# Kernel optimization log

Measured on AMD Instinct MI355X. Metric: run time of the kernel, lower is better.

Reference implementation:

```python
import jax, jax.numpy as jnp
import numpy as np

# angular momenta of the full basis (2s,3s,2p,3p,3d) -> block sizes 1,1,3,3,5; norb=13
L_LIST = [0, 0, 1, 1, 2]


def factor_matrix():
    """Replicates the orbital-pair loop: factor 0.5 on diagonal orbital blocks,
    1.0 for i<j blocks, 0.0 below the block diagonal (only i<=j filled)."""
    sizes = [2 * l + 1 for l in L_LIST]
    norb = sum(sizes)
    F = np.zeros((norb, norb), np.float32)
    ist = 0
    for i, si in enumerate(sizes):
        jst = 0
        for j, sj in enumerate(sizes):
            if i < j:
                F[ist:ist + si, jst:jst + sj] = 1.0
            elif i == j:
                F[ist:ist + si, jst:jst + sj] = 0.5
            jst += sj
        ist += si
    return jnp.asarray(F)


def setup_inputs() -> dict:
    key = jax.random.key(0)
    k1, k2, k3, k4, k5 = jax.random.split(key, 5)
    N, E, K = 128, 2048, 16
    norb = sum(2 * l + 1 for l in L_LIST)  # 13
    return {
        "hopping": jax.random.normal(k1, (E, norb * norb), jnp.float32),
        "onsite": jax.random.normal(k2, (N, norb * norb), jnp.float32),
        "kpoints": jax.random.uniform(k3, (K, 3), jnp.float32),
        "cell_shift": jax.random.normal(k4, (E, 3), jnp.float32),
        "edge_index": jax.random.randint(k5, (2, E), 0, N, jnp.int64),
    }


def reference(hopping, onsite, kpoints, cell_shift, edge_index):
    F = factor_matrix()
    norb = F.shape[0]
    N = onsite.shape[0]
    K = kpoints.shape[0]
    ctype = jnp.complex64

    # per-edge / per-atom orbital blocks with upper-triangular factor (i<=j loop)
    hop = (hopping.reshape(-1, norb, norb) * F).astype(ctype)   # [E,norb,norb]
    ons = (onsite.reshape(-1, norb, norb) * F).astype(ctype)    # [N,norb,norb]

    # Bloch phase exp(-i 2*pi k.R) per (k, edge)
    phase = jnp.exp(-1j * 2.0 * jnp.pi * (kpoints @ cell_shift.T).astype(ctype))  # [K,E]

    # assemble block Hamiltonian [K, N, N, norb, norb]
    H = jnp.zeros((K, N, N, norb, norb), ctype)
    ar = jnp.arange(N)
    H = H.at[:, ar, ar].add(ons[None])  # onsite diagonal blocks (no phase)
    ie, je = edge_index[0], edge_index[1]
    H = H.at[:, ie, je].add(phase[:, :, None, None] * hop[None])  # scatter-add edges

    # hermitize: block + block^H (swap atom blocks and orbital indices)
    H = H + jnp.conj(jnp.swapaxes(jnp.swapaxes(H, 1, 2), 3, 4))
    # [K, N, norb, N, norb] -> [K, all_norb, all_norb]
    Hk = H.transpose(0, 1, 3, 2, 4).reshape(K, N * norb, N * norb)
    return Hk
```

## Files before the change

kernel.cpp:

```cpp
#include <hip/hip_runtime.h>
#include <math.h>

#define NORB 13
#define NORB2 (NORB * NORB)
#define GB 16
#define NCOL (GB * NORB)
#define KSPLIT 2
#define MAXE 128
#define NTHR 256

typedef float fx2 __attribute__((ext_vector_type(2)));

__device__ __forceinline__ int blk_of(int p) {
    return p < 1 ? 0 : (p < 2 ? 1 : (p < 5 ? 2 : (p < 8 ? 3 : 4)));
}
__device__ __forceinline__ float bfac(int bp, int bq) {
    return bp < bq ? 1.0f : (bp == bq ? 0.5f : 0.0f);
}

__global__ void __launch_bounds__(NTHR)
k_fused(const float* __restrict__ hopping,
        const float* __restrict__ onsite,
        const float* __restrict__ kpoints,
        const float* __restrict__ cell_shift,
        const int* __restrict__ edge_index,
        float* __restrict__ out,
        int N, int E, int K, int ld, int es, int ngroups) {
    int g  = blockIdx.x % ngroups;
    int a  = (blockIdx.x / ngroups) % N;
    int kc = blockIdx.x / (ngroups * N);
    int kch = (K + KSPLIT - 1) / KSPLIT;
    int k0 = kc * kch, k1 = min(K, k0 + kch);
    int tid = threadIdx.x;
    int b0 = g * GB;

    __shared__ int ecnt;
    __shared__ int list[MAXE];

    if (tid == 0) ecnt = 0;
    __syncthreads();

    for (int e = tid; e < E; e += NTHR) {
        int ie = edge_index[e], je = edge_index[E + e];
        if (ie == a && (je >> 4) == g) {
            int pos = atomicAdd(&ecnt, 1);
            if (pos < MAXE) list[pos] = (e << 5) | ((je & 15) << 1);
        }
        if (je == a && (ie >> 4) == g) {
            int pos = atomicAdd(&ecnt, 1);
            if (pos < MAXE) list[pos] = (e << 5) | ((ie & 15) << 1) | 1;
        }
    }
    __syncthreads();
    int nent = min(__builtin_amdgcn_readfirstlane(ecnt), MAXE);

    int lane = tid & 63;
    int myent = (lane < nent) ? list[lane] : 0;

    int c = tid;
    if (c >= NCOL || g * NCOL + c >= ld) return;
    int i_c = c / NORB;
    int q   = c - i_c * NORB;
    int bq  = blk_of(q);
    bool diagact = (b0 + i_c == a);
    const float* on = onsite + (size_t)a * NORB2;

    for (int k = k0; k < k1; ++k) {
        float kx = kpoints[3 * k], ky = kpoints[3 * k + 1], kz = kpoints[3 * k + 2];

        float ax[NORB], ay[NORB];
        #pragma unroll
        for (int p = 0; p < NORB; ++p) {
            float v = 0.f;
            if (diagact) {
                int bp = blk_of(p);
                v = on[p * NORB + q] * bfac(bp, bq)
                  + on[q * NORB + p] * bfac(bq, bp);
            }
            ax[p] = v; ay[p] = 0.f;
        }

        for (int it = 0; it < nent; ++it) {
            int ent = (it < 64) ? __builtin_amdgcn_readlane(myent, it) : list[it];
            int e = ent >> 5;
            int islot = (ent >> 1) & 15;
            int rev = ent & 1;
            const float* cs = cell_shift + 3 * (size_t)e;
            float d = kx * cs[0] + ky * cs[1] + kz * cs[2];
            float s, cc;
            __sincosf(-6.2831853071795864f * d, &s, &cc);
            float sv = rev ? -s : s;
            if (i_c == islot) {
                const float* h = hopping + (size_t)e * NORB2;
                if (rev) {
                    #pragma unroll
                    for (int p = 0; p < NORB; ++p) {
                        float hv = h[q * NORB + p] * bfac(bq, blk_of(p));
                        ax[p] += cc * hv; ay[p] += sv * hv;
                    }
                } else {
                    #pragma unroll
                    for (int p = 0; p < NORB; ++p) {
                        float hv = h[p * NORB + q] * bfac(blk_of(p), bq);
                        ax[p] += cc * hv; ay[p] += sv * hv;
                    }
                }
            }
        }

        size_t base = ((size_t)(k * ld + a * NORB)) * ld + (size_t)g * NCOL + c;
        if (es == 2) {
            fx2* o2 = (fx2*)out;
            #pragma unroll
            for (int p = 0; p < NORB; ++p)
                o2[base + (size_t)p * ld] = (fx2){ax[p], ay[p]};
        } else {
            #pragma unroll
            for (int p = 0; p < NORB; ++p)
                out[base + (size_t)p * ld] = ax[p];
        }
    }
}

extern "C" void kernel_launch(void* const* d_in, const int* in_sizes, int n_in,
                              void* d_out, int out_size, void* d_ws, size_t ws_size,
                              hipStream_t stream) {
    const float* hopping    = (const float*)d_in[0];
    const float* onsite     = (const float*)d_in[1];
    const float* kpoints    = (const float*)d_in[2];
    const float* cell_shift = (const float*)d_in[3];
    const int*   edge_index = (const int*)d_in[4];
    float* out = (float*)d_out;

    int E = in_sizes[0] / NORB2;
    int N = in_sizes[1] / NORB2;
    int K = in_sizes[2] / 3;
    int ld = N * NORB;
    int ngroups = (N + GB - 1) / GB;

    size_t full = (size_t)K * ld * ld * 2;
    int es = ((size_t)out_size >= full) ? 2 : 1;

    int nwg = N * ngroups * KSPLIT;
    k_fused<<<nwg, NTHR, 0, stream>>>(hopping, onsite, kpoints, cell_shift,
                                      edge_index, out, N, E, K, ld, es, ngroups);
}
```

Before: 207.9 us.

## Map one workgroup per (k, atom) row with two columns per thread

Reorganises the grid so each workgroup of 832 threads handles a full block-row for one k-point and atom, with each thread owning two adjacent output columns. Phases are computed once per edge into shared memory instead of per thread per edge, and stores become 16-byte vector writes of two complex values. This removes the per-column-group edge rescans and redundant sincos work, at the cost of more registers per thread and larger workgroups.

```diff
diff --git a/kernel.cpp b/kernel.cpp
--- a/kernel.cpp
+++ b/kernel.cpp
@@ -3,13 +3,11 @@
 
 #define NORB 13
 #define NORB2 (NORB * NORB)
-#define GB 16
-#define NCOL (GB * NORB)
-#define KSPLIT 2
-#define MAXE 128
-#define NTHR 256
+#define NTHR 832
+#define MAXE 256
 
 typedef float fx2 __attribute__((ext_vector_type(2)));
+typedef float fx4 __attribute__((ext_vector_type(4)));
 
 __device__ __forceinline__ int blk_of(int p) {
     return p < 1 ? 0 : (p < 2 ? 1 : (p < 5 ? 2 : (p < 8 ? 3 : 4)));
@@ -25,99 +23,112 @@
         const float* __restrict__ cell_shift,
         const int* __restrict__ edge_index,
         float* __restrict__ out,
-        int N, int E, int K, int ld, int es, int ngroups) {
-    int g  = blockIdx.x % ngroups;
-    int a  = (blockIdx.x / ngroups) % N;
-    int kc = blockIdx.x / (ngroups * N);
-    int kch = (K + KSPLIT - 1) / KSPLIT;
-    int k0 = kc * kch, k1 = min(K, k0 + kch);
+        int N, int E, int K, int ld, int es) {
+    int a = blockIdx.x % N;
+    int k = blockIdx.x / N;
     int tid = threadIdx.x;
-    int b0 = g * GB;
 
     __shared__ int ecnt;
-    __shared__ int list[MAXE];
+    __shared__ int   elist[MAXE];
+    __shared__ float phc[MAXE];
+    __shared__ float phs[MAXE];
 
     if (tid == 0) ecnt = 0;
     __syncthreads();
 
     for (int e = tid; e < E; e += NTHR) {
         int ie = edge_index[e], je = edge_index[E + e];
-        if (ie == a && (je >> 4) == g) {
-            int pos = atomicAdd(&ecnt, 1);
-            if (pos < MAXE) list[pos] = (e << 5) | ((je & 15) << 1);
-        }
-        if (je == a && (ie >> 4) == g) {
-            int pos = atomicAdd(&ecnt, 1);
-            if (pos < MAXE) list[pos] = (e << 5) | ((ie & 15) << 1) | 1;
-        }
+        if (ie == a) { int pos = atomicAdd(&ecnt, 1);
+                       if (pos < MAXE) elist[pos] = (e << 8) | (je << 1); }
+        if (je == a) { int pos = atomicAdd(&ecnt, 1);
+                       if (pos < MAXE) elist[pos] = (e << 8) | (ie << 1) | 1; }
     }
     __syncthreads();
     int nent = min(__builtin_amdgcn_readfirstlane(ecnt), MAXE);
 
+    float kx = kpoints[3 * k], ky = kpoints[3 * k + 1], kz = kpoints[3 * k + 2];
+    for (int t = tid; t < nent; t += NTHR) {
+        int ent = elist[t];
+        int e = ent >> 8;
+        float d = kx * cell_shift[3 * e] + ky * cell_shift[3 * e + 1]
+                + kz * cell_shift[3 * e + 2];
+        float s, c;
+        __sincosf(-6.2831853071795864f * d, &s, &c);
+        phc[t] = c;
+        phs[t] = (ent & 1) ? -s : s;
+    }
+    __syncthreads();
+
     int lane = tid & 63;
-    int myent = (lane < nent) ? list[lane] : 0;
+    int   bent = (lane < nent) ? elist[lane] : 0;
+    float bc   = (lane < nent) ? phc[lane]  : 0.f;
+    float bs   = (lane < nent) ? phs[lane]  : 0.f;
 
-    int c = tid;
-    if (c >= NCOL || g * NCOL + c >= ld) return;
-    int i_c = c / NORB;
-    int q   = c - i_c * NORB;
-    int bq  = blk_of(q);
-    bool diagact = (b0 + i_c == a);
+    int c0 = 2 * tid, c1 = c0 + 1;
+    int b0a = c0 / NORB, q0 = c0 - NORB * b0a;
+    int b1a = c1 / NORB, q1 = c1 - NORB * b1a;
+    int bq0 = blk_of(q0), bq1 = blk_of(q1);
+
+    float a0x[NORB], a0y[NORB], a1x[NORB], a1y[NORB];
     const float* on = onsite + (size_t)a * NORB2;
+    #pragma unroll
+    for (int p = 0; p < NORB; ++p) {
+        int bp = blk_of(p);
+        float v0 = 0.f, v1 = 0.f;
+        if (b0a == a) v0 = on[p * NORB + q0] * bfac(bp, bq0)
+                         + on[q0 * NORB + p] * bfac(bq0, bp);
+        if (b1a == a) v1 = on[p * NORB + q1] * bfac(bp, bq1)
+                         + on[q1 * NORB + p] * bfac(bq1, bp);
+        a0x[p] = v0; a0y[p] = 0.f;
+        a1x[p] = v1; a1y[p] = 0.f;
+    }
 
-    for (int k = k0; k < k1; ++k) {
-        float kx = kpoints[3 * k], ky = kpoints[3 * k + 1], kz = kpoints[3 * k + 2];
+    for (int it = 0; it < nent; ++it) {
+        int ent; float cc, ss;
+        if (it < 64) {
+            ent = __builtin_amdgcn_readlane(bent, it);
+            cc  = __int_as_float(__builtin_amdgcn_readlane(__float_as_int(bc), it));
+            ss  = __int_as_float(__builtin_amdgcn_readlane(__float_as_int(bs), it));
+        } else {
+            ent = elist[it]; cc = phc[it]; ss = phs[it];
+        }
+        int bb  = (ent >> 1) & 127;
+        int rev = ent & 1;
+        const float* h = hopping + (size_t)(ent >> 8) * NORB2;
+        if (b0a == bb) {
+            #pragma unroll
+            for (int p = 0; p < NORB; ++p) {
+                int bp = blk_of(p);
+                float hv = rev ? h[q0 * NORB + p] * bfac(bq0, bp)
+                               : h[p * NORB + q0] * bfac(bp, bq0);
+                a0x[p] += cc * hv; a0y[p] += ss * hv;
+            }
+        }
+        if (b1a == bb) {
+            #pragma unroll
+            for (int p = 0; p < NORB; ++p) {
+                int bp = blk_of(p);
+                float hv = rev ? h[q1 * NORB + p] * bfac(bq1, bp)
+                               : h[p * NORB + q1] * bfac(bp, bq1);
+                a1x[p] += cc * hv; a1y[p] += ss * hv;
+            }
+        }
+    }
 
-        float ax[NORB], ay[NORB];
+    size_t rowbase = ((size_t)(k * ld + a * NORB)) * ld;
+    if (es == 2) {
+        fx4* o4 = (fx4*)out;
         #pragma unroll
         for (int p = 0; p < NORB; ++p) {
-            float v = 0.f;
-            if (diagact) {
-                int bp = blk_of(p);
-                v = on[p * NORB + q] * bfac(bp, bq)
-                  + on[q * NORB + p] * bfac(bq, bp);
-            }
-            ax[p] = v; ay[p] = 0.f;
+            size_t ci = rowbase + (size_t)p * ld + c0;
+            o4[ci >> 1] = (fx4){a0x[p], a0y[p], a1x[p], a1y[p]};
         }
-
-        for (int it = 0; it < nent; ++it) {
-            int ent = (it < 64) ? __builtin_amdgcn_readlane(myent, it) : list[it];
-            int e = ent >> 5;
-            int islot = (ent >> 1) & 15;
-            int rev = ent & 1;
-            const float* cs = cell_shift + 3 * (size_t)e;
-            float d = kx * cs[0] + ky * cs[1] + kz * cs[2];
-            float s, cc;
-            __sincosf(-6.2831853071795864f * d, &s, &cc);
-            float sv = rev ? -s : s;
-            if (i_c == islot) {
-                const float* h = hopping + (size_t)e * NORB2;
-                if (rev) {
-                    #pragma unroll
-                    for (int p = 0; p < NORB; ++p) {
-                        float hv = h[q * NORB + p] * bfac(bq, blk_of(p));
-                        ax[p] += cc * hv; ay[p] += sv * hv;
-                    }
-                } else {
-                    #pragma unroll
-                    for (int p = 0; p < NORB; ++p) {
-                        float hv = h[p * NORB + q] * bfac(blk_of(p), bq);
-                        ax[p] += cc * hv; ay[p] += sv * hv;
-                    }
-                }
-            }
-        }
-
-        size_t base = ((size_t)(k * ld + a * NORB)) * ld + (size_t)g * NCOL + c;
-        if (es == 2) {
-            fx2* o2 = (fx2*)out;
-            #pragma unroll
-            for (int p = 0; p < NORB; ++p)
-                o2[base + (size_t)p * ld] = (fx2){ax[p], ay[p]};
-        } else {
-            #pragma unroll
-            for (int p = 0; p < NORB; ++p)
-                out[base + (size_t)p * ld] = ax[p];
+    } else {
+        fx2* o2 = (fx2*)out;
+        #pragma unroll
+        for (int p = 0; p < NORB; ++p) {
+            size_t ci = rowbase + (size_t)p * ld + c0;
+            o2[ci >> 1] = (fx2){a0x[p], a1x[p]};
         }
     }
 }
@@ -136,12 +147,11 @@
     int N = in_sizes[1] / NORB2;
     int K = in_sizes[2] / 3;
     int ld = N * NORB;
-    int ngroups = (N + GB - 1) / GB;
 
     size_t full = (size_t)K * ld * ld * 2;
     int es = ((size_t)out_size >= full) ? 2 : 1;
 
-    int nwg = N * ngroups * KSPLIT;
+    int nwg = N * K;
     k_fused<<<nwg, NTHR, 0, stream>>>(hopping, onsite, kpoints, cell_shift,
-                                      edge_index, out, N, E, K, ld, es, ngroups);
+                                      edge_index, out, N, E, K, ld, es);
 }
```

After: 317.0 us. +52.4%, slower.
